# Kernel optimization log

Measured on AMD Instinct MI355X. Metric: run time of the kernel, lower is better.

## Reference

```python
import jax, jax.numpy as jnp
import numpy as np

N, E, D, H = 100000, 400000, 128, 128  # nodes, edges, feat dim, mlp hidden


def _ln(x, g, b, eps=1e-5):
    m = jnp.mean(x, axis=-1, keepdims=True)
    v = jnp.mean((x - m) ** 2, axis=-1, keepdims=True)
    return (x - m) * jax.lax.rsqrt(v + eps) * g + b


def _mlp(x, w0, b0, w1, b1, w2, b2):
    # Linear->ReLU->Linear->ReLU->Linear (last act = Identity)
    h = jax.nn.relu(x @ w0 + b0)
    h = jax.nn.relu(h @ w1 + b1)
    return h @ w2 + b2


def setup_inputs() -> dict:
    key = jax.random.key(0)
    ks = jax.random.split(key, 16)
    node_x = jax.random.normal(ks[0], (N, D), dtype=jnp.float32)
    edge_attr = jax.random.normal(ks[1], (E, D), dtype=jnp.float32)
    edge_index = jax.random.randint(ks[2], (2, E), 0, N, dtype=jnp.int32)

    def lin(k, fin, fout):
        kw, kb = jax.random.split(k)
        s = 1.0 / np.sqrt(fin)
        w = jax.random.uniform(kw, (fin, fout), jnp.float32, -s, s)
        b = jax.random.uniform(kb, (fout,), jnp.float32, -s, s)
        return w, b

    # message MLP: (3D) -> H -> H -> D, then LayerNorm(D)
    msg_w0, msg_b0 = lin(ks[3], 3 * D, H)
    msg_w1, msg_b1 = lin(ks[4], H, H)
    msg_w2, msg_b2 = lin(ks[5], H, D)
    # top-level update MLP: (D + D) -> H -> H -> D, then LayerNorm(D)
    upd_w0, upd_b0 = lin(ks[6], 2 * D, H)
    upd_w1, upd_b1 = lin(ks[7], H, H)
    upd_w2, upd_b2 = lin(ks[8], H, D)
    return {
        "node_x": node_x, "edge_attr": edge_attr, "edge_index": edge_index,
        "msg_w0": msg_w0, "msg_b0": msg_b0, "msg_w1": msg_w1, "msg_b1": msg_b1,
        "msg_w2": msg_w2, "msg_b2": msg_b2,
        "msg_g": jnp.ones((D,), jnp.float32), "msg_beta": jnp.zeros((D,), jnp.float32),
        "upd_w0": upd_w0, "upd_b0": upd_b0, "upd_w1": upd_w1, "upd_b1": upd_b1,
        "upd_w2": upd_w2, "upd_b2": upd_b2,
        "upd_g": jnp.ones((D,), jnp.float32), "upd_beta": jnp.zeros((D,), jnp.float32),
    }


def reference(node_x, edge_attr, edge_index,
              msg_w0, msg_b0, msg_w1, msg_b1, msg_w2, msg_b2, msg_g, msg_beta,
              upd_w0, upd_b0, upd_w1, upd_b1, upd_w2, upd_b2, upd_g, upd_beta):
    src, dst = edge_index[0], edge_index[1]
    # PyG default flow source_to_target: x_j = x[src], x_i = x[dst]
    x_i = node_x[dst]                       # [E, D]
    x_j = node_x[src]                       # [E, D]
    concat = jnp.concatenate([x_i, x_j, edge_attr], axis=1)  # [E, 3D]
    msg = _ln(_mlp(concat, msg_w0, msg_b0, msg_w1, msg_b1, msg_w2, msg_b2), msg_g, msg_beta)
    new_edge = edge_attr + msg              # edge_attr[:] += msg in original
    # scatter-add messages onto target nodes
    agg = jax.ops.segment_sum(new_edge, dst, num_segments=N)  # [N, D]
    concat2 = jnp.concatenate([node_x, agg], axis=1)          # [N, 2D]
    upd = _ln(_mlp(concat2, upd_w0, upd_b0, upd_w1, upd_b1, upd_w2, upd_b2), upd_g, upd_beta)
    return node_x + upd
```

## Files before the change

kernel.cpp:

```cpp
#include <hip/hip_runtime.h>

typedef __attribute__((ext_vector_type(4))) float f32x4;
typedef __attribute__((ext_vector_type(8))) __bf16 bf16x8;

constexpr int FD = 128;

__device__ __forceinline__ uint4 pack8(const float* v) {
  union { __bf16 h[8]; uint4 u; } cv;
#pragma unroll
  for (int q = 0; q < 8; ++q) cv.h[q] = (__bf16)v[q];
  return cv.u;
}
__device__ __forceinline__ unsigned int pack2(float a, float b) {
  union { __bf16 h[2]; unsigned int u; } cv;
  cv.h[0] = (__bf16)a; cv.h[1] = (__bf16)b;
  return cv.u;
}

__global__ void cvt_bf16(const float* __restrict__ x, unsigned short* __restrict__ o, int n8) {
  int i = blockIdx.x * 256 + threadIdx.x;
  if (i >= n8) return;
  const float* p = x + (size_t)i * 8;
  float v[8];
#pragma unroll
  for (int q = 0; q < 8; ++q) v[q] = p[q];
  *(uint4*)(o + (size_t)i * 8) = pack8(v);
}

__global__ void pack_weights(const float* __restrict__ mw0, const float* __restrict__ mw1,
                             const float* __restrict__ mw2, const float* __restrict__ uw0,
                             const float* __restrict__ uw1, const float* __restrict__ uw2,
                             unsigned short* __restrict__ wp) {
  int tid = blockIdx.x * 256 + threadIdx.x;
  const float* src; int base, K;
  if      (tid < 49152)  { src = mw0; base = 0;      K = 384; }
  else if (tid < 65536)  { src = mw1; base = 49152;  K = 128; }
  else if (tid < 81920)  { src = mw2; base = 65536;  K = 128; }
  else if (tid < 114688) { src = uw0; base = 81920;  K = 256; }
  else if (tid < 131072) { src = uw1; base = 114688; K = 128; }
  else                   { src = uw2; base = 131072; K = 128; }
  int i = tid - base;
  int k = i >> 7, n = i & 127;
  int KS = K >> 5;
  int dst = base + (((n >> 4) * KS + (k >> 5)) * 64 + ((k >> 3) & 3) * 16 + (n & 15)) * 8 + (k & 7);
  union { __bf16 h; unsigned short s; } cv; cv.h = (__bf16)src[i];
  wp[dst] = cv.s;
}


template<bool RELU>
__device__ __forceinline__ void store_frag(unsigned short* sDst, const f32x4* acc, float bias) {
#pragma unroll
  for (int m = 0; m < 4; ++m)
#pragma unroll
    for (int ri = 0; ri < 4; ++ri) {
      float v = acc[m][ri] + bias;
      if (RELU) v = fmaxf(v, 0.f);
      union { __bf16 h; unsigned short s; } cv; cv.h = (__bf16)v;
      sDst[m * 512 + ri * 32] = cv.s;
    }
}

__global__ __launch_bounds__(512, 6)
void in_edge_kernel(const float* __restrict__ node_x, const unsigned short* __restrict__ nxbf,
                    const float* __restrict__ edge_attr,
                    const int* __restrict__ eidx, const unsigned short* __restrict__ wp,
                    const float* __restrict__ b0p, const float* __restrict__ b1p,
                    const float* __restrict__ b2p, const float* __restrict__ gp,
                    const float* __restrict__ bep,
                    unsigned short* __restrict__ msg, int* __restrict__ head,
                    int* __restrict__ nxt, float* __restrict__ agg,
                    int use_sort, int E) {
  __shared__ unsigned short sBuf[3072 * 8];
  __shared__ int sSrc[64], sDst[64];
  __shared__ float sG[128], sB[128];

  const int t = threadIdx.x;
  const int e0 = blockIdx.x * 64;
  const int lane = t & 63, w = t >> 6;
  const int ln = lane & 15, g16 = lane >> 4;
  const int col = w * 16 + ln;
  const int rdoff = ln * 32 + g16 * 8;
  const int stoff = (w >> 1) * 2048 + g16 * 128
                  + (((2 * w) + (ln >> 3)) & 3) * 8 + (ln & 7);

  bf16x8 b0[6];
#pragma unroll
  for (int ks = 0; ks < 6; ++ks)
    b0[ks] = *(const bf16x8*)(wp + (size_t)((w * 12 + ks) * 64 + lane) * 8);
  bf16x8 B1r[4];
#pragma unroll
  for (int ks = 0; ks < 4; ++ks)
    B1r[ks] = *(const bf16x8*)(wp + 49152 + (size_t)((w * 4 + ks) * 64 + lane) * 8);

  if (t < 64) {
    sSrc[t] = (e0 + t < E) ? eidx[e0 + t] : 0;
  } else if (t < 128) {
    int r = t - 64;
    int e = e0 + r;
    int d = (e < E) ? eidx[E + e] : 0;
    sDst[r] = d;
    if (use_sort && e < E) nxt[e] = atomicExch(&head[d], e);
  } else if (t < 256) {
    sG[t - 128] = gp[t - 128];
  } else if (t < 384) {
    sB[t - 256] = bep[t - 256];
  }
  __syncthreads();

  if (nxbf) {
#pragma unroll
    for (int it = 0; it < 2; ++it) {
      int f = t + it * 512;
      int row = f >> 4, j = f & 15;
      uint4 v = {0, 0, 0, 0}, u = {0, 0, 0, 0};
      if (e0 + row < E) {
        v = *(const uint4*)(nxbf + (size_t)sDst[row] * FD + j * 8);
        u = *(const uint4*)(nxbf + (size_t)sSrc[row] * FD + j * 8);
      }
      int c = (((j >> 2) * 4 + (row >> 4)) * 64 + (row & 15) * 4 + (j & 3)) * 8;
      *(uint4*)&sBuf[c] = v;
      *(uint4*)&sBuf[c + 8192] = u;
    }
  } else {
#pragma unroll
    for (int it = 0; it < 16; ++it) {
      const int type = it >> 3;
      int row = ((it & 7) << 3) + w;
      float2 v = {0.f, 0.f};
      if (e0 + row < E) {
        const float* sp = (type == 0) ? node_x + (size_t)sDst[row] * FD
                                      : node_x + (size_t)sSrc[row] * FD;
        v = *(const float2*)(sp + lane * 2);
      }
      int c = (((type * 4 + (lane >> 4)) * 4 + (row >> 4)) * 64
               + (row & 15) * 4 + ((lane >> 2) & 3)) * 8 + (lane & 3) * 2;
      *(unsigned int*)&sBuf[c] = pack2(v.x, v.y);
    }
  }
#pragma unroll
  for (int it = 0; it < 8; ++it) {
    int row = it * 8 + w;
    float2 v = {0.f, 0.f};
    if (e0 + row < E) v = *(const float2*)(edge_attr + (size_t)(e0 + row) * FD + lane * 2);
    int c = 16384 + (((lane >> 4) * 4 + (row >> 4)) * 64
                     + (row & 15) * 4 + ((lane >> 2) & 3)) * 8 + (lane & 3) * 2;
    *(unsigned int*)&sBuf[c] = pack2(v.x, v.y);
  }
  __syncthreads();

  const float b0v = b0p[col], b1v = b1p[col], b2v = b2p[col];

  f32x4 acc[4];
#pragma unroll
  for (int m = 0; m < 4; ++m) acc[m] = (f32x4){0.f, 0.f, 0.f, 0.f};

#pragma unroll
  for (int ks = 0; ks < 12; ++ks) {
    bf16x8 bb = b0[ks % 6];
    if (ks + 6 < 12)
      b0[ks % 6] = *(const bf16x8*)(wp + (size_t)((w * 12 + ks + 6) * 64 + lane) * 8);
#pragma unroll
    for (int m = 0; m < 4; ++m) {
      bf16x8 a = *(const bf16x8*)&sBuf[(ks * 4 + m) * 512 + rdoff];
      acc[m] = __builtin_amdgcn_mfma_f32_16x16x32_bf16(a, bb, acc[m], 0, 0, 0);
    }
  }
  bf16x8 B2r[4];
#pragma unroll
  for (int ks = 0; ks < 4; ++ks)
    B2r[ks] = *(const bf16x8*)(wp + 65536 + (size_t)((w * 4 + ks) * 64 + lane) * 8);

  __syncthreads();
  store_frag<true>(sBuf + stoff, acc, b0v);
  __syncthreads();

#pragma unroll
  for (int m = 0; m < 4; ++m) acc[m] = (f32x4){0.f, 0.f, 0.f, 0.f};
#pragma unroll
  for (int ks = 0; ks < 4; ++ks)
#pragma unroll
    for (int m = 0; m < 4; ++m) {
      bf16x8 a = *(const bf16x8*)&sBuf[(ks * 4 + m) * 512 + rdoff];
      acc[m] = __builtin_amdgcn_mfma_f32_16x16x32_bf16(a, B1r[ks], acc[m], 0, 0, 0);
    }
  store_frag<true>(sBuf + 8192 + stoff, acc, b1v);
  __syncthreads();

#pragma unroll
  for (int m = 0; m < 4; ++m) acc[m] = (f32x4){0.f, 0.f, 0.f, 0.f};
#pragma unroll
  for (int ks = 0; ks < 4; ++ks)
#pragma unroll
    for (int m = 0; m < 4; ++m) {
      bf16x8 a = *(const bf16x8*)&sBuf[8192 + (ks * 4 + m) * 512 + rdoff];
      acc[m] = __builtin_amdgcn_mfma_f32_16x16x32_bf16(a, B2r[ks], acc[m], 0, 0, 0);
    }
  store_frag<false>(sBuf + stoff, acc, b2v);
  __syncthreads();

  {
    int row = t >> 3, j = t & 7;
    int a0 = (((j >> 1) * 4 + (row >> 4)) * 64 + (row & 15) * 4 + 2 * (j & 1)) * 8;
    bf16x8 v0 = *(const bf16x8*)&sBuf[a0];
    bf16x8 v1 = *(const bf16x8*)&sBuf[a0 + 8];
    float s1 = 0.f, s2 = 0.f;
#pragma unroll
    for (int q = 0; q < 8; ++q) {
      float a = (float)v0[q], b = (float)v1[q];
      s1 += a + b; s2 += a * a + b * b;
    }
#pragma unroll
    for (int m = 1; m < 8; m <<= 1) {
      s1 += __shfl_xor(s1, m, 64);
      s2 += __shfl_xor(s2, m, 64);
    }
    float mean = s1 * (1.f / 128.f);
    float var  = s2 * (1.f / 128.f) - mean * mean;
    float rstd = rsqrtf(fmaxf(var, 0.f) + 1e-5f);

    int e = e0 + row;
    if (e < E) {
      bf16x8 ea0 = *(const bf16x8*)&sBuf[a0 + 16384];
      bf16x8 ea1 = *(const bf16x8*)&sBuf[a0 + 16384 + 8];
      float val[16];
#pragma unroll
      for (int q = 0; q < 8; ++q) {
        val[q]     = ((float)v0[q] - mean) * rstd * sG[j * 16 + q]     + sB[j * 16 + q]     + (float)ea0[q];
        val[8 + q] = ((float)v1[q] - mean) * rstd * sG[j * 16 + 8 + q] + sB[j * 16 + 8 + q] + (float)ea1[q];
      }
      if (use_sort) {
        uint4* dst = (uint4*)(msg + (size_t)e * FD + j * 16);
        dst[0] = pack8(val);
        dst[1] = pack8(val + 8);
      } else {
        float* ap = agg + (size_t)sDst[row] * FD + j * 16;
#pragma unroll
        for (int q = 0; q < 16; ++q) atomicAdd(ap + q, val[q]);
      }
    }
  }
}

__global__ __launch_bounds__(512, 8)
void in_node_kernel(const float* __restrict__ node_x, const unsigned short* __restrict__ nxbf,
                    const unsigned short* __restrict__ msg, const int* __restrict__ head,
                    const int* __restrict__ nxt, const float* __restrict__ agg,
                    const unsigned short* __restrict__ wp,
                    const float* __restrict__ b0p, const float* __restrict__ b1p,
                    const float* __restrict__ b2p, const float* __restrict__ gp,
                    const float* __restrict__ bep, float* __restrict__ out,
                    int use_sort, int N) {
  __shared__ unsigned short sBuf[2048 * 8];
  __shared__ float sG[128], sB[128];

  const int t = threadIdx.x;
  const int r0 = blockIdx.x * 64;
  const int lane = t & 63, w = t >> 6;
  const int ln = lane & 15, g16 = lane >> 4;
  const int col = w * 16 + ln;
  const int rdoff = ln * 32 + g16 * 8;
  const int stoff = (w >> 1) * 2048 + g16 * 128
                  + (((2 * w) + (ln >> 3)) & 3) * 8 + (ln & 7);

  bf16x8 b0[4];
#pragma unroll
  for (int ks = 0; ks < 4; ++ks)
    b0[ks] = *(const bf16x8*)(wp + 81920 + (size_t)((w * 8 + ks) * 64 + lane) * 8);

  if (t < 128)      sG[t] = gp[t];
  else if (t < 256) sB[t - 128] = bep[t - 128];

  if (nxbf) {
#pragma unroll
    for (int it = 0; it < 2; ++it) {
      int f = t + it * 512;
      int row = f >> 4, j = f & 15;
      int r = r0 + row;
      uint4 v = {0, 0, 0, 0};
      if (r < N) v = *(const uint4*)(nxbf + (size_t)r * FD + j * 8);
      int c = (((j >> 2) * 4 + (row >> 4)) * 64 + (row & 15) * 4 + (j & 3)) * 8;
      *(uint4*)&sBuf[c] = v;
    }
  } else {
#pragma unroll
    for (int it = 0; it < 8; ++it) {
      int row = (it << 3) + w;
      int r = r0 + row;
      float2 v = {0.f, 0.f};
      if (r < N) v = *(const float2*)(node_x + (size_t)r * FD + lane * 2);
      int c = (((lane >> 4) * 4 + (row >> 4)) * 64
               + (row & 15) * 4 + ((lane >> 2) & 3)) * 8 + (lane & 3) * 2;
      *(unsigned int*)&sBuf[c] = pack2(v.x, v.y);
    }
  }

  {
    int row = t >> 3, j = t & 7;
    int node = r0 + row;
    float a[16];
#pragma unroll
    for (int q = 0; q < 16; ++q) a[q] = 0.f;
    if (node < N) {
      if (use_sort) {
        int e = head[node];
        while (e >= 0) {
          int ne = nxt[e];
          bf16x8 m0 = *(const bf16x8*)(msg + (size_t)e * FD + j * 16);
          bf16x8 m1 = *(const bf16x8*)(msg + (size_t)e * FD + j * 16 + 8);
#pragma unroll
          for (int q = 0; q < 8; ++q) { a[q] += (float)m0[q]; a[8 + q] += (float)m1[q]; }
          e = ne;
        }
      } else {
        const float* ap = agg + (size_t)node * FD + j * 16;
#pragma unroll
        for (int q4 = 0; q4 < 4; ++q4) {
          f32x4 u = *(const f32x4*)(ap + q4 * 4);
#pragma unroll
          for (int q = 0; q < 4; ++q) a[q4 * 4 + q] = u[q];
        }
      }
    }
    int c = 8192 + (((j >> 1) * 4 + (row >> 4)) * 64 + (row & 15) * 4 + 2 * (j & 1)) * 8;
    *(uint4*)&sBuf[c] = pack8(a);
    *(uint4*)&sBuf[c + 8] = pack8(a + 8);
  }
  __syncthreads();

  const float b0v = b0p[col], b1v = b1p[col], b2v = b2p[col];

  f32x4 acc[4];
#pragma unroll
  for (int m = 0; m < 4; ++m) acc[m] = (f32x4){0.f, 0.f, 0.f, 0.f};

#pragma unroll
  for (int ks = 0; ks < 8; ++ks) {
    bf16x8 bb = b0[ks % 4];
    if (ks + 4 < 8)
      b0[ks % 4] = *(const bf16x8*)(wp + 81920 + (size_t)((w * 8 + ks + 4) * 64 + lane) * 8);
#pragma unroll
    for (int m = 0; m < 4; ++m) {
      bf16x8 a = *(const bf16x8*)&sBuf[(ks * 4 + m) * 512 + rdoff];
      acc[m] = __builtin_amdgcn_mfma_f32_16x16x32_bf16(a, bb, acc[m], 0, 0, 0);
    }
  }
  bf16x8 B1r[4];
#pragma unroll
  for (int ks = 0; ks < 4; ++ks)
    B1r[ks] = *(const bf16x8*)(wp + 114688 + (size_t)((w * 4 + ks) * 64 + lane) * 8);

  __syncthreads();
  store_frag<true>(sBuf + stoff, acc, b0v);
  __syncthreads();

#pragma unroll
  for (int m = 0; m < 4; ++m) acc[m] = (f32x4){0.f, 0.f, 0.f, 0.f};
#pragma unroll
  for (int ks = 0; ks < 4; ++ks)
#pragma unroll
    for (int m = 0; m < 4; ++m) {
      bf16x8 a = *(const bf16x8*)&sBuf[(ks * 4 + m) * 512 + rdoff];
      acc[m] = __builtin_amdgcn_mfma_f32_16x16x32_bf16(a, B1r[ks], acc[m], 0, 0, 0);
    }
  bf16x8 B2r[4];
#pragma unroll
  for (int ks = 0; ks < 4; ++ks)
    B2r[ks] = *(const bf16x8*)(wp + 131072 + (size_t)((w * 4 + ks) * 64 + lane) * 8);
  store_frag<true>(sBuf + 8192 + stoff, acc, b1v);
  __syncthreads();

#pragma unroll
  for (int m = 0; m < 4; ++m) acc[m] = (f32x4){0.f, 0.f, 0.f, 0.f};
#pragma unroll
  for (int ks = 0; ks < 4; ++ks)
#pragma unroll
    for (int m = 0; m < 4; ++m) {
      bf16x8 a = *(const bf16x8*)&sBuf[8192 + (ks * 4 + m) * 512 + rdoff];
      acc[m] = __builtin_amdgcn_mfma_f32_16x16x32_bf16(a, B2r[ks], acc[m], 0, 0, 0);
    }
  store_frag<false>(sBuf + stoff, acc, b2v);
  __syncthreads();

  {
    int row = t >> 3, j = t & 7;
    int a0 = (((j >> 1) * 4 + (row >> 4)) * 64 + (row & 15) * 4 + 2 * (j & 1)) * 8;
    bf16x8 v0 = *(const bf16x8*)&sBuf[a0];
    bf16x8 v1 = *(const bf16x8*)&sBuf[a0 + 8];
    float s1 = 0.f, s2 = 0.f;
#pragma unroll
    for (int q = 0; q < 8; ++q) {
      float a = (float)v0[q], b = (float)v1[q];
      s1 += a + b; s2 += a * a + b * b;
    }
#pragma unroll
    for (int m = 1; m < 8; m <<= 1) {
      s1 += __shfl_xor(s1, m, 64);
      s2 += __shfl_xor(s2, m, 64);
    }
    float mean = s1 * (1.f / 128.f);
    float var  = s2 * (1.f / 128.f) - mean * mean;
    float rstd = rsqrtf(fmaxf(var, 0.f) + 1e-5f);

    int node = r0 + row;
    if (node < N) {
      float o[16];
#pragma unroll
      for (int q = 0; q < 8; ++q) {
        o[q]     = ((float)v0[q] - mean) * rstd * sG[j * 16 + q]     + sB[j * 16 + q];
        o[8 + q] = ((float)v1[q] - mean) * rstd * sG[j * 16 + 8 + q] + sB[j * 16 + 8 + q];
      }
      const float* xr = node_x + (size_t)node * FD + j * 16;
      float* orow = out + (size_t)node * FD + j * 16;
#pragma unroll
      for (int q4 = 0; q4 < 4; ++q4) {
        f32x4 x = *(const f32x4*)(xr + q4 * 4);
        f32x4 wv;
#pragma unroll
        for (int q = 0; q < 4; ++q) wv[q] = o[q4 * 4 + q] + x[q];
        *(f32x4*)(orow + q4 * 4) = wv;
      }
    }
  }
}

extern "C" void kernel_launch(void* const* d_in, const int* in_sizes, int n_in,
                              void* d_out, int out_size, void* d_ws, size_t ws_size,
                              hipStream_t stream) {
  const float* node_x    = (const float*)d_in[0];
  const float* edge_attr = (const float*)d_in[1];
  const int*   eidx      = (const int*)d_in[2];
  const int N = in_sizes[0] / FD;
  const int E = in_sizes[1] / FD;

  char* ws = (char*)d_ws;
  auto aln = [](size_t x) { return (x + 255) & ~(size_t)255; };
  const size_t wpB   = aln(294912);
  const size_t nxbfB = aln((size_t)N * FD * 2);
  const size_t headB = aln((size_t)N * 4);
  const size_t nxtB  = aln((size_t)E * 4);
  const size_t msgB  = (size_t)E * FD * 2;

  unsigned short* wp = (unsigned short*)ws;
  unsigned short* nxbf = nullptr;
  int* head = nullptr; int* nxt = nullptr;
  unsigned short* msg = nullptr; float* agg = nullptr;
  int use_sort = 0;

  if (ws_size >= wpB + nxbfB + headB + nxtB + msgB) {
    use_sort = 1;
    nxbf = (unsigned short*)(ws + wpB);
    head = (int*)(ws + wpB + nxbfB);
    nxt  = (int*)(ws + wpB + nxbfB + headB);
    msg  = (unsigned short*)(ws + wpB + nxbfB + headB + nxtB);
  } else if (ws_size >= wpB + headB + nxtB + msgB) {
    use_sort = 1;
    head = (int*)(ws + wpB);
    nxt  = (int*)(ws + wpB + headB);
    msg  = (unsigned short*)(ws + wpB + headB + nxtB);
  } else {
    agg = (float*)(ws + wpB);
  }

  if (use_sort) (void)hipMemsetAsync(head, 0xFF, (size_t)N * 4, stream);
  else          (void)hipMemsetAsync(agg, 0, (size_t)N * FD * sizeof(float), stream);

  pack_weights<<<576, 256, 0, stream>>>(
      (const float*)d_in[3], (const float*)d_in[5], (const float*)d_in[7],
      (const float*)d_in[11], (const float*)d_in[13], (const float*)d_in[15], wp);
  if (nxbf) cvt_bf16<<<(N * FD / 8 + 255) / 256, 256, 0, stream>>>(node_x, nxbf, N * FD / 8);
  in_edge_kernel<<<(E + 63) / 64, 512, 0, stream>>>(
      node_x, nxbf, edge_attr, eidx, wp,
      (const float*)d_in[4], (const float*)d_in[6], (const float*)d_in[8],
      (const float*)d_in[9], (const float*)d_in[10],
      msg, head, nxt, agg, use_sort, E);
  in_node_kernel<<<(N + 63) / 64, 512, 0, stream>>>(
      node_x, nxbf, msg, head, nxt, agg, wp,
      (const float*)d_in[12], (const float*)d_in[14], (const float*)d_in[16],
      (const float*)d_in[17], (const float*)d_in[18], (float*)d_out, use_sort, N);
}
```

Baseline: 239.4 us.

## Swizzle edge-kernel LDS layout, widen gathers, shrink weight prefetch, raise MFMA priority

Measured after the change: 300.1 us. 1.25x slower.

```diff
diff --git a/kernel.cpp b/kernel.cpp
--- a/kernel.cpp
+++ b/kernel.cpp
@@ -11,10 +11,11 @@
   for (int q = 0; q < 8; ++q) cv.h[q] = (__bf16)v[q];
   return cv.u;
 }
-__device__ __forceinline__ unsigned int pack2(float a, float b) {
-  union { __bf16 h[2]; unsigned int u; } cv;
-  cv.h[0] = (__bf16)a; cv.h[1] = (__bf16)b;
-  return cv.u;
+__device__ __forceinline__ uint4 pack8v(const f32x4 a, const f32x4 b) {
+  float v[8];
+#pragma unroll
+  for (int q = 0; q < 4; ++q) { v[q] = a[q]; v[4 + q] = b[q]; }
+  return pack8(v);
 }
 
 __global__ void cvt_bf16(const float* __restrict__ x, unsigned short* __restrict__ o, int n8) {
@@ -48,19 +49,6 @@
 }
 
 
-template<bool RELU>
-__device__ __forceinline__ void store_frag(unsigned short* sDst, const f32x4* acc, float bias) {
-#pragma unroll
-  for (int m = 0; m < 4; ++m)
-#pragma unroll
-    for (int ri = 0; ri < 4; ++ri) {
-      float v = acc[m][ri] + bias;
-      if (RELU) v = fmaxf(v, 0.f);
-      union { __bf16 h; unsigned short s; } cv; cv.h = (__bf16)v;
-      sDst[m * 512 + ri * 32] = cv.s;
-    }
-}
-
 __global__ __launch_bounds__(512, 6)
 void in_edge_kernel(const float* __restrict__ node_x, const unsigned short* __restrict__ nxbf,
                     const float* __restrict__ edge_attr,
@@ -79,19 +67,17 @@
   const int e0 = blockIdx.x * 64;
   const int lane = t & 63, w = t >> 6;
   const int ln = lane & 15, g16 = lane >> 4;
-  const int col = w * 16 + ln;
-  const int rdoff = ln * 32 + g16 * 8;
-  const int stoff = (w >> 1) * 2048 + g16 * 128
-                  + (((2 * w) + (ln >> 3)) & 3) * 8 + (ln & 7);
-
-  bf16x8 b0[6];
-#pragma unroll
-  for (int ks = 0; ks < 6; ++ks)
-    b0[ks] = *(const bf16x8*)(wp + (size_t)((w * 12 + ks) * 64 + lane) * 8);
-  bf16x8 B1r[4];
-#pragma unroll
-  for (int ks = 0; ks < 4; ++ks)
-    B1r[ks] = *(const bf16x8*)(wp + 49152 + (size_t)((w * 4 + ks) * 64 + lane) * 8);
+  const int ql = ln * 4 + g16;
+  const int keyw = (w >> 1) & 3;
+  const int stoffX = g16 * 128 + ((((2 * w) + (ln >> 3)) & 3) ^ keyw) * 8 + (ln & 7);
+
+  bf16x8 bx[4], B1r[4];
+#pragma unroll
+  for (int k = 0; k < 4; ++k)
+    bx[k] = *(const bf16x8*)(wp + (size_t)((w * 12 + k) * 64 + lane) * 8);
+#pragma unroll
+  for (int k = 0; k < 4; ++k)
+    B1r[k] = *(const bf16x8*)(wp + 49152 + (size_t)((w * 4 + k) * 64 + lane) * 8);
 
   if (t < 64) {
     sSrc[t] = (e0 + t < E) ? eidx[e0 + t] : 0;
@@ -109,101 +95,146 @@
   __syncthreads();
 
   if (nxbf) {
+    int sel = w >> 2;
+    int row = (w * 16 + (lane >> 2)) & 63;
+    int tt = lane & 3;
+    const int* idxp = sel ? sSrc : sDst;
+    uint4 v[4] = {{0,0,0,0},{0,0,0,0},{0,0,0,0},{0,0,0,0}};
+    if (e0 + row < E) {
+      const unsigned short* sp = nxbf + (size_t)idxp[row] * FD + tt * 32;
+#pragma unroll
+      for (int i = 0; i < 4; ++i) v[i] = *(const uint4*)(sp + i * 8);
+    }
+    int grp = tt * 4 + (row >> 4);
+    int base = sel * 8192 + grp * 512 + (row & 15) * 32;
+#pragma unroll
+    for (int i = 0; i < 4; ++i)
+      *(uint4*)&sBuf[base + ((i ^ tt) * 8)] = v[i];
+  } else {
 #pragma unroll
     for (int it = 0; it < 2; ++it) {
-      int f = t + it * 512;
-      int row = f >> 4, j = f & 15;
-      uint4 v = {0, 0, 0, 0}, u = {0, 0, 0, 0};
+      int sel = w >> 2;
+      int row = (w * 16 + (lane >> 2)) & 63;
+      int seg = (lane & 3) + it * 4;
+      const int* idxp = sel ? sSrc : sDst;
+      f32x4 f[4] = {{0,0,0,0},{0,0,0,0},{0,0,0,0},{0,0,0,0}};
       if (e0 + row < E) {
-        v = *(const uint4*)(nxbf + (size_t)sDst[row] * FD + j * 8);
-        u = *(const uint4*)(nxbf + (size_t)sSrc[row] * FD + j * 8);
-      }
-      int c = (((j >> 2) * 4 + (row >> 4)) * 64 + (row & 15) * 4 + (j & 3)) * 8;
-      *(uint4*)&sBuf[c] = v;
-      *(uint4*)&sBuf[c + 8192] = u;
-    }
-  } else {
-#pragma unroll
-    for (int it = 0; it < 16; ++it) {
-      const int type = it >> 3;
-      int row = ((it & 7) << 3) + w;
-      float2 v = {0.f, 0.f};
-      if (e0 + row < E) {
-        const float* sp = (type == 0) ? node_x + (size_t)sDst[row] * FD
-                                      : node_x + (size_t)sSrc[row] * FD;
-        v = *(const float2*)(sp + lane * 2);
-      }
-      int c = (((type * 4 + (lane >> 4)) * 4 + (row >> 4)) * 64
-               + (row & 15) * 4 + ((lane >> 2) & 3)) * 8 + (lane & 3) * 2;
-      *(unsigned int*)&sBuf[c] = pack2(v.x, v.y);
-    }
-  }
-#pragma unroll
-  for (int it = 0; it < 8; ++it) {
-    int row = it * 8 + w;
-    float2 v = {0.f, 0.f};
-    if (e0 + row < E) v = *(const float2*)(edge_attr + (size_t)(e0 + row) * FD + lane * 2);
-    int c = 16384 + (((lane >> 4) * 4 + (row >> 4)) * 64
-                     + (row & 15) * 4 + ((lane >> 2) & 3)) * 8 + (lane & 3) * 2;
-    *(unsigned int*)&sBuf[c] = pack2(v.x, v.y);
-  }
-  __syncthreads();
-
+        const float* sp = node_x + (size_t)idxp[row] * FD + seg * 16;
+#pragma unroll
+        for (int i = 0; i < 4; ++i) f[i] = *(const f32x4*)(sp + i * 4);
+      }
+      int jc = seg * 2;
+      int grp = (jc >> 2) * 4 + (row >> 4);
+      int key = (grp >> 2) & 3;
+      int tb = sel * 8192 + grp * 512;
+      int q0 = (row & 15) * 4 + (jc & 3);
+      *(uint4*)&sBuf[tb + ((q0 ^ key) * 8)]       = pack8v(f[0], f[1]);
+      *(uint4*)&sBuf[tb + (((q0 + 1) ^ key) * 8)] = pack8v(f[2], f[3]);
+    }
+  }
+  {
+    int row = t >> 3, seg = t & 7;
+    f32x4 f[4] = {{0,0,0,0},{0,0,0,0},{0,0,0,0},{0,0,0,0}};
+    if (e0 + row < E) {
+      const float* sp = edge_attr + (size_t)(e0 + row) * FD + seg * 16;
+#pragma unroll
+      for (int i = 0; i < 4; ++i) f[i] = *(const f32x4*)(sp + i * 4);
+    }
+    int jc = seg * 2;
+    int grp = (jc >> 2) * 4 + (row >> 4);
+    int key = (grp >> 2) & 3;
+    int tb = 16384 + grp * 512;
+    int q0 = (row & 15) * 4 + (jc & 3);
+    *(uint4*)&sBuf[tb + ((q0 ^ key) * 8)]       = pack8v(f[0], f[1]);
+    *(uint4*)&sBuf[tb + (((q0 + 1) ^ key) * 8)] = pack8v(f[2], f[3]);
+  }
+  __syncthreads();
+
+  const int col = w * 16 + ln;
   const float b0v = b0p[col], b1v = b1p[col], b2v = b2p[col];
 
   f32x4 acc[4];
 #pragma unroll
   for (int m = 0; m < 4; ++m) acc[m] = (f32x4){0.f, 0.f, 0.f, 0.f};
 
+  __builtin_amdgcn_s_setprio(1);
 #pragma unroll
   for (int ks = 0; ks < 12; ++ks) {
-    bf16x8 bb = b0[ks % 6];
-    if (ks + 6 < 12)
-      b0[ks % 6] = *(const bf16x8*)(wp + (size_t)((w * 12 + ks + 6) * 64 + lane) * 8);
+    bf16x8 bb = bx[ks & 3];
+    if (ks + 4 < 12)
+      bx[ks & 3] = *(const bf16x8*)(wp + (size_t)((w * 12 + ks + 4) * 64 + lane) * 8);
 #pragma unroll
     for (int m = 0; m < 4; ++m) {
-      bf16x8 a = *(const bf16x8*)&sBuf[(ks * 4 + m) * 512 + rdoff];
+      bf16x8 a = *(const bf16x8*)&sBuf[(ks * 4 + m) * 512 + ((ql ^ (ks & 3)) * 8)];
       acc[m] = __builtin_amdgcn_mfma_f32_16x16x32_bf16(a, bb, acc[m], 0, 0, 0);
     }
   }
-  bf16x8 B2r[4];
-#pragma unroll
-  for (int ks = 0; ks < 4; ++ks)
-    B2r[ks] = *(const bf16x8*)(wp + 65536 + (size_t)((w * 4 + ks) * 64 + lane) * 8);
-
-  __syncthreads();
-  store_frag<true>(sBuf + stoff, acc, b0v);
-  __syncthreads();
-
-#pragma unroll
-  for (int m = 0; m < 4; ++m) acc[m] = (f32x4){0.f, 0.f, 0.f, 0.f};
+  __builtin_amdgcn_s_setprio(0);
+#pragma unroll
+  for (int k = 0; k < 4; ++k)
+    bx[k] = *(const bf16x8*)(wp + 65536 + (size_t)((w * 4 + k) * 64 + lane) * 8);
+  __syncthreads();
+
+#pragma unroll
+  for (int m = 0; m < 4; ++m)
+#pragma unroll
+    for (int ri = 0; ri < 4; ++ri) {
+      union { __bf16 h; unsigned short s; } cv;
+      cv.h = (__bf16)fmaxf(acc[m][ri] + b0v, 0.f);
+      sBuf[((w >> 1) * 4 + m) * 512 + ri * 32 + stoffX] = cv.s;
+      acc[m][ri] = 0.f;
+    }
+  __syncthreads();
+
+  __builtin_amdgcn_s_setprio(1);
 #pragma unroll
   for (int ks = 0; ks < 4; ++ks)
 #pragma unroll
     for (int m = 0; m < 4; ++m) {
-      bf16x8 a = *(const bf16x8*)&sBuf[(ks * 4 + m) * 512 + rdoff];
+      bf16x8 a = *(const bf16x8*)&sBuf[(ks * 4 + m) * 512 + ((ql ^ ks) * 8)];
       acc[m] = __builtin_amdgcn_mfma_f32_16x16x32_bf16(a, B1r[ks], acc[m], 0, 0, 0);
     }
-  store_frag<true>(sBuf + 8192 + stoff, acc, b1v);
-  __syncthreads();
-
-#pragma unroll
-  for (int m = 0; m < 4; ++m) acc[m] = (f32x4){0.f, 0.f, 0.f, 0.f};
+  __builtin_amdgcn_s_setprio(0);
+#pragma unroll
+  for (int m = 0; m < 4; ++m)
+#pragma unroll
+    for (int ri = 0; ri < 4; ++ri) {
+      union { __bf16 h; unsigned short s; } cv;
+      cv.h = (__bf16)fmaxf(acc[m][ri] + b1v, 0.f);
+      sBuf[8192 + ((w >> 1) * 4 + m) * 512 + ri * 32 + stoffX] = cv.s;
+      acc[m][ri] = 0.f;
+    }
+  __syncthreads();
+
+  __builtin_amdgcn_s_setprio(1);
 #pragma unroll
   for (int ks = 0; ks < 4; ++ks)
 #pragma unroll
     for (int m = 0; m < 4; ++m) {
-      bf16x8 a = *(const bf16x8*)&sBuf[8192 + (ks * 4 + m) * 512 + rdoff];
-      acc[m] = __builtin_amdgcn_mfma_f32_16x16x32_bf16(a, B2r[ks], acc[m], 0, 0, 0);
-    }
-  store_frag<false>(sBuf + stoff, acc, b2v);
+      bf16x8 a = *(const bf16x8*)&sBuf[8192 + (ks * 4 + m) * 512 + ((ql ^ ks) * 8)];
+      acc[m] = __builtin_amdgcn_mfma_f32_16x16x32_bf16(a, bx[ks], acc[m], 0, 0, 0);
+    }
+  __builtin_amdgcn_s_setprio(0);
+#pragma unroll
+  for (int m = 0; m < 4; ++m)
+#pragma unroll
+    for (int ri = 0; ri < 4; ++ri) {
+      union { __bf16 h; unsigned short s; } cv;
+      cv.h = (__bf16)(acc[m][ri] + b2v);
+      sBuf[((w >> 1) * 4 + m) * 512 + ri * 32 + stoffX] = cv.s;
+    }
   __syncthreads();
 
   {
     int row = t >> 3, j = t & 7;
-    int a0 = (((j >> 1) * 4 + (row >> 4)) * 64 + (row & 15) * 4 + 2 * (j & 1)) * 8;
+    int grp = (j >> 1) * 4 + (row >> 4);
+    int key = (j >> 1) & 3;
+    int qa = ((row & 15) * 4 + 2 * (j & 1)) ^ key;
+    int qb = ((row & 15) * 4 + 2 * (j & 1) + 1) ^ key;
+    int a0 = grp * 512 + qa * 8;
+    int a1 = grp * 512 + qb * 8;
     bf16x8 v0 = *(const bf16x8*)&sBuf[a0];
-    bf16x8 v1 = *(const bf16x8*)&sBuf[a0 + 8];
+    bf16x8 v1 = *(const bf16x8*)&sBuf[a1];
     float s1 = 0.f, s2 = 0.f;
 #pragma unroll
     for (int q = 0; q < 8; ++q) {
@@ -221,8 +252,8 @@
 
     int e = e0 + row;
     if (e < E) {
-      bf16x8 ea0 = *(const bf16x8*)&sBuf[a0 + 16384];
-      bf16x8 ea1 = *(const bf16x8*)&sBuf[a0 + 16384 + 8];
+      bf16x8 ea0 = *(const bf16x8*)&sBuf[16384 + a0];
+      bf16x8 ea1 = *(const bf16x8*)&sBuf[16384 + a1];
       float val[16];
 #pragma unroll
       for (int q = 0; q < 8; ++q) {
@@ -284,14 +315,17 @@
     }
   } else {
 #pragma unroll
-    for (int it = 0; it < 8; ++it) {
-      int row = (it << 3) + w;
+    for (int it = 0; it < 2; ++it) {
+      int f = t + it * 512;
+      int row = f >> 4, j = f & 15;
       int r = r0 + row;
-      float2 v = {0.f, 0.f};
-      if (r < N) v = *(const float2*)(node_x + (size_t)r * FD + lane * 2);
-      int c = (((lane >> 4) * 4 + (row >> 4)) * 64
-               + (row & 15) * 4 + ((lane >> 2) & 3)) * 8 + (lane & 3) * 2;
-      *(unsigned int*)&sBuf[c] = pack2(v.x, v.y);
+      f32x4 fa = {0,0,0,0}, fb = {0,0,0,0};
+      if (r < N) {
+        fa = *(const f32x4*)(node_x + (size_t)r * FD + j * 8);
+        fb = *(const f32x4*)(node_x + (size_t)r * FD + j * 8 + 4);
+      }
+      int c = (((j >> 2) * 4 + (row >> 4)) * 64 + (row & 15) * 4 + (j & 3)) * 8;
+      *(uint4*)&sBuf[c] = pack8v(fa, fb);
     }
   }
 
@@ -351,11 +385,17 @@
     B1r[ks] = *(const bf16x8*)(wp + 114688 + (size_t)((w * 4 + ks) * 64 + lane) * 8);
 
   __syncthreads();
-  store_frag<true>(sBuf + stoff, acc, b0v);
-  __syncthreads();
-
-#pragma unroll
-  for (int m = 0; m < 4; ++m) acc[m] = (f32x4){0.f, 0.f, 0.f, 0.f};
+#pragma unroll
+  for (int m = 0; m < 4; ++m)
+#pragma unroll
+    for (int ri = 0; ri < 4; ++ri) {
+      union { __bf16 h; unsigned short s; } cv;
+      cv.h = (__bf16)fmaxf(acc[m][ri] + b0v, 0.f);
+      sBuf[stoff + m * 512 + ri * 32] = cv.s;
+      acc[m][ri] = 0.f;
+    }
+  __syncthreads();
+
 #pragma unroll
   for (int ks = 0; ks < 4; ++ks)
 #pragma unroll
@@ -367,11 +407,17 @@
 #pragma unroll
   for (int ks = 0; ks < 4; ++ks)
     B2r[ks] = *(const bf16x8*)(wp + 131072 + (size_t)((w * 4 + ks) * 64 + lane) * 8);
-  store_frag<true>(sBuf + 8192 + stoff, acc, b1v);
-  __syncthreads();
-
-#pragma unroll
-  for (int m = 0; m < 4; ++m) acc[m] = (f32x4){0.f, 0.f, 0.f, 0.f};
+#pragma unroll
+  for (int m = 0; m < 4; ++m)
+#pragma unroll
+    for (int ri = 0; ri < 4; ++ri) {
+      union { __bf16 h; unsigned short s; } cv;
+      cv.h = (__bf16)fmaxf(acc[m][ri] + b1v, 0.f);
+      sBuf[8192 + stoff + m * 512 + ri * 32] = cv.s;
+      acc[m][ri] = 0.f;
+    }
+  __syncthreads();
+
 #pragma unroll
   for (int ks = 0; ks < 4; ++ks)
 #pragma unroll
@@ -379,7 +425,14 @@
       bf16x8 a = *(const bf16x8*)&sBuf[8192 + (ks * 4 + m) * 512 + rdoff];
       acc[m] = __builtin_amdgcn_mfma_f32_16x16x32_bf16(a, B2r[ks], acc[m], 0, 0, 0);
     }
-  store_frag<false>(sBuf + stoff, acc, b2v);
+#pragma unroll
+  for (int m = 0; m < 4; ++m)
+#pragma unroll
+    for (int ri = 0; ri < 4; ++ri) {
+      union { __bf16 h; unsigned short s; } cv;
+      cv.h = (__bf16)(acc[m][ri] + b2v);
+      sBuf[stoff + m * 512 + ri * 32] = cv.s;
+    }
   __syncthreads();
 
   {
```

## Restructure edge MLP as register-resident swapped GEMM with shuffle-based layer transitions

Applied to the files above, without the earlier changes.

Result: slower. 424.7 us (+77.4%).

```diff
diff --git a/kernel.cpp b/kernel.cpp
--- a/kernel.cpp
+++ b/kernel.cpp
@@ -2,20 +2,26 @@
 
 typedef __attribute__((ext_vector_type(4))) float f32x4;
 typedef __attribute__((ext_vector_type(8))) __bf16 bf16x8;
+typedef unsigned int u32;
 
 constexpr int FD = 128;
 
+__device__ __forceinline__ u32 pk2(float a, float b) {
+  union { __bf16 h[2]; u32 u; } cv; cv.h[0] = (__bf16)a; cv.h[1] = (__bf16)b; return cv.u;
+}
+__device__ __forceinline__ bf16x8 mk8(u32 a, u32 b, u32 c, u32 d) {
+  union { u32 w[4]; bf16x8 v; } cv; cv.w[0] = a; cv.w[1] = b; cv.w[2] = c; cv.w[3] = d; return cv.v;
+}
+__device__ __forceinline__ bf16x8 pack8f(const f32x4 a, const f32x4 b) {
+  return mk8(pk2(a[0], a[1]), pk2(a[2], a[3]), pk2(b[0], b[1]), pk2(b[2], b[3]));
+}
 __device__ __forceinline__ uint4 pack8(const float* v) {
   union { __bf16 h[8]; uint4 u; } cv;
 #pragma unroll
   for (int q = 0; q < 8; ++q) cv.h[q] = (__bf16)v[q];
   return cv.u;
 }
-__device__ __forceinline__ unsigned int pack2(float a, float b) {
-  union { __bf16 h[2]; unsigned int u; } cv;
-  cv.h[0] = (__bf16)a; cv.h[1] = (__bf16)b;
-  return cv.u;
-}
+__device__ __forceinline__ unsigned int pack2(float a, float b) { return pk2(a, b); }
 
 __global__ void cvt_bf16(const float* __restrict__ x, unsigned short* __restrict__ o, int n8) {
   int i = blockIdx.x * 256 + threadIdx.x;
@@ -47,21 +53,7 @@
   wp[dst] = cv.s;
 }
 
-
-template<bool RELU>
-__device__ __forceinline__ void store_frag(unsigned short* sDst, const f32x4* acc, float bias) {
-#pragma unroll
-  for (int m = 0; m < 4; ++m)
-#pragma unroll
-    for (int ri = 0; ri < 4; ++ri) {
-      float v = acc[m][ri] + bias;
-      if (RELU) v = fmaxf(v, 0.f);
-      union { __bf16 h; unsigned short s; } cv; cv.h = (__bf16)v;
-      sDst[m * 512 + ri * 32] = cv.s;
-    }
-}
-
-__global__ __launch_bounds__(512, 6)
+__global__ __launch_bounds__(256, 4)
 void in_edge_kernel(const float* __restrict__ node_x, const unsigned short* __restrict__ nxbf,
                     const float* __restrict__ edge_attr,
                     const int* __restrict__ eidx, const unsigned short* __restrict__ wp,
@@ -71,172 +63,173 @@
                     unsigned short* __restrict__ msg, int* __restrict__ head,
                     int* __restrict__ nxt, float* __restrict__ agg,
                     int use_sort, int E) {
-  __shared__ unsigned short sBuf[3072 * 8];
-  __shared__ int sSrc[64], sDst[64];
-  __shared__ float sG[128], sB[128];
+  __shared__ float sP[5][128];
 
   const int t = threadIdx.x;
-  const int e0 = blockIdx.x * 64;
   const int lane = t & 63, w = t >> 6;
   const int ln = lane & 15, g16 = lane >> 4;
-  const int col = w * 16 + ln;
-  const int rdoff = ln * 32 + g16 * 8;
-  const int stoff = (w >> 1) * 2048 + g16 * 128
-                  + (((2 * w) + (ln >> 3)) & 3) * 8 + (ln & 7);
-
-  bf16x8 b0[6];
-#pragma unroll
-  for (int ks = 0; ks < 6; ++ks)
-    b0[ks] = *(const bf16x8*)(wp + (size_t)((w * 12 + ks) * 64 + lane) * 8);
-  bf16x8 B1r[4];
-#pragma unroll
-  for (int ks = 0; ks < 4; ++ks)
-    B1r[ks] = *(const bf16x8*)(wp + 49152 + (size_t)((w * 4 + ks) * 64 + lane) * 8);
-
-  if (t < 64) {
-    sSrc[t] = (e0 + t < E) ? eidx[e0 + t] : 0;
-  } else if (t < 128) {
-    int r = t - 64;
-    int e = e0 + r;
-    int d = (e < E) ? eidx[E + e] : 0;
-    sDst[r] = d;
-    if (use_sort && e < E) nxt[e] = atomicExch(&head[d], e);
-  } else if (t < 256) {
-    sG[t - 128] = gp[t - 128];
-  } else if (t < 384) {
-    sB[t - 256] = bep[t - 256];
-  }
-  __syncthreads();
-
-  if (nxbf) {
-#pragma unroll
-    for (int it = 0; it < 2; ++it) {
-      int f = t + it * 512;
-      int row = f >> 4, j = f & 15;
-      uint4 v = {0, 0, 0, 0}, u = {0, 0, 0, 0};
-      if (e0 + row < E) {
-        v = *(const uint4*)(nxbf + (size_t)sDst[row] * FD + j * 8);
-        u = *(const uint4*)(nxbf + (size_t)sSrc[row] * FD + j * 8);
-      }
-      int c = (((j >> 2) * 4 + (row >> 4)) * 64 + (row & 15) * 4 + (j & 3)) * 8;
-      *(uint4*)&sBuf[c] = v;
-      *(uint4*)&sBuf[c + 8192] = u;
-    }
-  } else {
-#pragma unroll
-    for (int it = 0; it < 16; ++it) {
-      const int type = it >> 3;
-      int row = ((it & 7) << 3) + w;
-      float2 v = {0.f, 0.f};
-      if (e0 + row < E) {
-        const float* sp = (type == 0) ? node_x + (size_t)sDst[row] * FD
-                                      : node_x + (size_t)sSrc[row] * FD;
-        v = *(const float2*)(sp + lane * 2);
-      }
-      int c = (((type * 4 + (lane >> 4)) * 4 + (row >> 4)) * 64
-               + (row & 15) * 4 + ((lane >> 2) & 3)) * 8 + (lane & 3) * 2;
-      *(unsigned int*)&sBuf[c] = pack2(v.x, v.y);
-    }
-  }
-#pragma unroll
-  for (int it = 0; it < 8; ++it) {
-    int row = it * 8 + w;
-    float2 v = {0.f, 0.f};
-    if (e0 + row < E) v = *(const float2*)(edge_attr + (size_t)(e0 + row) * FD + lane * 2);
-    int c = 16384 + (((lane >> 4) * 4 + (row >> 4)) * 64
-                     + (row & 15) * 4 + ((lane >> 2) & 3)) * 8 + (lane & 3) * 2;
-    *(unsigned int*)&sBuf[c] = pack2(v.x, v.y);
-  }
-  __syncthreads();
-
-  const float b0v = b0p[col], b1v = b1p[col], b2v = b2p[col];
-
-  f32x4 acc[4];
-#pragma unroll
-  for (int m = 0; m < 4; ++m) acc[m] = (f32x4){0.f, 0.f, 0.f, 0.f};
-
-#pragma unroll
-  for (int ks = 0; ks < 12; ++ks) {
-    bf16x8 bb = b0[ks % 6];
-    if (ks + 6 < 12)
-      b0[ks % 6] = *(const bf16x8*)(wp + (size_t)((w * 12 + ks + 6) * 64 + lane) * 8);
-#pragma unroll
-    for (int m = 0; m < 4; ++m) {
-      bf16x8 a = *(const bf16x8*)&sBuf[(ks * 4 + m) * 512 + rdoff];
-      acc[m] = __builtin_amdgcn_mfma_f32_16x16x32_bf16(a, bb, acc[m], 0, 0, 0);
-    }
-  }
-  bf16x8 B2r[4];
-#pragma unroll
-  for (int ks = 0; ks < 4; ++ks)
-    B2r[ks] = *(const bf16x8*)(wp + 65536 + (size_t)((w * 4 + ks) * 64 + lane) * 8);
-
-  __syncthreads();
-  store_frag<true>(sBuf + stoff, acc, b0v);
-  __syncthreads();
-
-#pragma unroll
-  for (int m = 0; m < 4; ++m) acc[m] = (f32x4){0.f, 0.f, 0.f, 0.f};
-#pragma unroll
-  for (int ks = 0; ks < 4; ++ks)
-#pragma unroll
-    for (int m = 0; m < 4; ++m) {
-      bf16x8 a = *(const bf16x8*)&sBuf[(ks * 4 + m) * 512 + rdoff];
-      acc[m] = __builtin_amdgcn_mfma_f32_16x16x32_bf16(a, B1r[ks], acc[m], 0, 0, 0);
-    }
-  store_frag<true>(sBuf + 8192 + stoff, acc, b1v);
-  __syncthreads();
-
-#pragma unroll
-  for (int m = 0; m < 4; ++m) acc[m] = (f32x4){0.f, 0.f, 0.f, 0.f};
-#pragma unroll
-  for (int ks = 0; ks < 4; ++ks)
-#pragma unroll
-    for (int m = 0; m < 4; ++m) {
-      bf16x8 a = *(const bf16x8*)&sBuf[8192 + (ks * 4 + m) * 512 + rdoff];
-      acc[m] = __builtin_amdgcn_mfma_f32_16x16x32_bf16(a, B2r[ks], acc[m], 0, 0, 0);
-    }
-  store_frag<false>(sBuf + stoff, acc, b2v);
-  __syncthreads();
-
-  {
-    int row = t >> 3, j = t & 7;
-    int a0 = (((j >> 1) * 4 + (row >> 4)) * 64 + (row & 15) * 4 + 2 * (j & 1)) * 8;
-    bf16x8 v0 = *(const bf16x8*)&sBuf[a0];
-    bf16x8 v1 = *(const bf16x8*)&sBuf[a0 + 8];
-    float s1 = 0.f, s2 = 0.f;
-#pragma unroll
-    for (int q = 0; q < 8; ++q) {
-      float a = (float)v0[q], b = (float)v1[q];
-      s1 += a + b; s2 += a * a + b * b;
-    }
-#pragma unroll
-    for (int m = 1; m < 8; m <<= 1) {
-      s1 += __shfl_xor(s1, m, 64);
-      s2 += __shfl_xor(s2, m, 64);
-    }
-    float mean = s1 * (1.f / 128.f);
-    float var  = s2 * (1.f / 128.f) - mean * mean;
-    float rstd = rsqrtf(fmaxf(var, 0.f) + 1e-5f);
-
-    int e = e0 + row;
-    if (e < E) {
-      bf16x8 ea0 = *(const bf16x8*)&sBuf[a0 + 16384];
-      bf16x8 ea1 = *(const bf16x8*)&sBuf[a0 + 16384 + 8];
-      float val[16];
-#pragma unroll
-      for (int q = 0; q < 8; ++q) {
-        val[q]     = ((float)v0[q] - mean) * rstd * sG[j * 16 + q]     + sB[j * 16 + q]     + (float)ea0[q];
-        val[8 + q] = ((float)v1[q] - mean) * rstd * sG[j * 16 + 8 + q] + sB[j * 16 + 8 + q] + (float)ea1[q];
-      }
-      if (use_sort) {
-        uint4* dst = (uint4*)(msg + (size_t)e * FD + j * 16);
-        dst[0] = pack8(val);
-        dst[1] = pack8(val + 8);
-      } else {
-        float* ap = agg + (size_t)sDst[row] * FD + j * 16;
-#pragma unroll
-        for (int q = 0; q < 16; ++q) atomicAdd(ap + q, val[q]);
+  const int e0w = blockIdx.x * 128 + w * 32;
+  const int erow0 = e0w + ln, erow1 = e0w + 16 + ln;
+  const int kg = 8 * g16;
+
+  int si0 = 0, si1 = 0, di0 = 0, di1 = 0;
+  if (erow0 < E) { si0 = eidx[erow0]; di0 = eidx[E + erow0]; }
+  if (erow1 < E) { si1 = eidx[erow1]; di1 = eidx[E + erow1]; }
+
+  if (t < 128) {
+    sP[0][t] = b0p[t]; sP[1][t] = b1p[t]; sP[2][t] = b2p[t];
+    sP[3][t] = gp[t];  sP[4][t] = bep[t];
+  }
+  if (use_sort && lane < 32) {
+    int e = e0w + lane;
+    if (e < E) { int d = (lane < 16) ? di0 : di1; nxt[e] = atomicExch(&head[d], e); }
+  }
+  __syncthreads();
+
+  auto xf = [&](int idx, int ko) -> bf16x8 {
+    if (nxbf) return *(const bf16x8*)(nxbf + (size_t)idx * FD + ko);
+    f32x4 a = *(const f32x4*)(node_x + (size_t)idx * FD + ko);
+    f32x4 b = *(const f32x4*)(node_x + (size_t)idx * FD + ko + 4);
+    return pack8f(a, b);
+  };
+  auto eaf = [&](int row, int ko) -> bf16x8 {
+    f32x4 a = {0.f,0.f,0.f,0.f}, b = {0.f,0.f,0.f,0.f};
+    if (row < E) {
+      a = *(const f32x4*)(edge_attr + (size_t)row * FD + ko);
+      b = *(const f32x4*)(edge_attr + (size_t)row * FD + ko + 4);
+    }
+    return pack8f(a, b);
+  };
+
+  bf16x8 rb[4][2];
+  auto loadkb = [&](int kb) {
+    int s = kb & 3;
+    if (kb < 4)      { int ko = kb * 32 + kg;       rb[s][0] = xf(di0, ko);     rb[s][1] = xf(di1, ko); }
+    else if (kb < 8) { int ko = (kb - 4) * 32 + kg; rb[s][0] = xf(si0, ko);     rb[s][1] = xf(si1, ko); }
+    else             { int ko = (kb - 8) * 32 + kg; rb[s][0] = eaf(erow0, ko);  rb[s][1] = eaf(erow1, ko); }
+  };
+
+  f32x4 acc[8][2];
+#pragma unroll
+  for (int mb = 0; mb < 8; ++mb)
+#pragma unroll
+    for (int nb = 0; nb < 2; ++nb) acc[mb][nb] = (f32x4){0.f, 0.f, 0.f, 0.f};
+
+  loadkb(0); loadkb(1); loadkb(2);
+
+#pragma unroll
+  for (int kb = 0; kb < 12; ++kb) {
+    if (kb + 3 < 12) loadkb(kb + 3);
+    const int s = kb & 3;
+#pragma unroll
+    for (int mb = 0; mb < 8; ++mb) {
+      bf16x8 a = *(const bf16x8*)(wp + (size_t)((mb * 12 + kb) * 64 + lane) * 8);
+      acc[mb][0] = __builtin_amdgcn_mfma_f32_16x16x32_bf16(a, rb[s][0], acc[mb][0], 0, 0, 0);
+      acc[mb][1] = __builtin_amdgcn_mfma_f32_16x16x32_bf16(a, rb[s][1], acc[mb][1], 0, 0, 0);
+    }
+  }
+
+  const int s0l = ln + ((g16 & 1) << 5);
+  const int s1l = s0l + 16;
+  const bool hi = g16 >= 2;
+  bf16x8 Bn[4][2];
+
+  auto transition = [&](int lyr) {
+    u32 clo[8][2], chi[8][2];
+#pragma unroll
+    for (int mb = 0; mb < 8; ++mb) {
+      f32x4 bv = *(const f32x4*)&sP[lyr][mb * 16 + 4 * g16];
+#pragma unroll
+      for (int nb = 0; nb < 2; ++nb) {
+        float v0 = fmaxf(acc[mb][nb][0] + bv[0], 0.f);
+        float v1 = fmaxf(acc[mb][nb][1] + bv[1], 0.f);
+        float v2 = fmaxf(acc[mb][nb][2] + bv[2], 0.f);
+        float v3 = fmaxf(acc[mb][nb][3] + bv[3], 0.f);
+        clo[mb][nb] = pk2(v0, v1); chi[mb][nb] = pk2(v2, v3);
+      }
+    }
+#pragma unroll
+    for (int kb = 0; kb < 4; ++kb)
+#pragma unroll
+      for (int nb = 0; nb < 2; ++nb) {
+        u32 a0 = __shfl((int)clo[2 * kb][nb], s0l, 64),     a1 = __shfl((int)chi[2 * kb][nb], s0l, 64);
+        u32 a2 = __shfl((int)clo[2 * kb][nb], s1l, 64),     a3 = __shfl((int)chi[2 * kb][nb], s1l, 64);
+        u32 b0 = __shfl((int)clo[2 * kb + 1][nb], s0l, 64), b1 = __shfl((int)chi[2 * kb + 1][nb], s0l, 64);
+        u32 b2 = __shfl((int)clo[2 * kb + 1][nb], s1l, 64), b3 = __shfl((int)chi[2 * kb + 1][nb], s1l, 64);
+        Bn[kb][nb] = mk8(hi ? b0 : a0, hi ? b1 : a1, hi ? b2 : a2, hi ? b3 : a3);
+      }
+#pragma unroll
+    for (int mb = 0; mb < 8; ++mb)
+#pragma unroll
+      for (int nb = 0; nb < 2; ++nb) acc[mb][nb] = (f32x4){0.f, 0.f, 0.f, 0.f};
+  };
+
+  transition(0);
+
+#pragma unroll
+  for (int kb = 0; kb < 4; ++kb)
+#pragma unroll
+    for (int mb = 0; mb < 8; ++mb) {
+      bf16x8 a = *(const bf16x8*)(wp + 49152 + (size_t)((mb * 4 + kb) * 64 + lane) * 8);
+      acc[mb][0] = __builtin_amdgcn_mfma_f32_16x16x32_bf16(a, Bn[kb][0], acc[mb][0], 0, 0, 0);
+      acc[mb][1] = __builtin_amdgcn_mfma_f32_16x16x32_bf16(a, Bn[kb][1], acc[mb][1], 0, 0, 0);
+    }
+
+  transition(1);
+
+#pragma unroll
+  for (int kb = 0; kb < 4; ++kb)
+#pragma unroll
+    for (int mb = 0; mb < 8; ++mb) {
+      bf16x8 a = *(const bf16x8*)(wp + 65536 + (size_t)((mb * 4 + kb) * 64 + lane) * 8);
+      acc[mb][0] = __builtin_amdgcn_mfma_f32_16x16x32_bf16(a, Bn[kb][0], acc[mb][0], 0, 0, 0);
+      acc[mb][1] = __builtin_amdgcn_mfma_f32_16x16x32_bf16(a, Bn[kb][1], acc[mb][1], 0, 0, 0);
+    }
+
+  float mean[2], rstd[2];
+#pragma unroll
+  for (int nb = 0; nb < 2; ++nb) {
+    float p = 0.f, q = 0.f;
+#pragma unroll
+    for (int mb = 0; mb < 8; ++mb) {
+      f32x4 bv = *(const f32x4*)&sP[2][mb * 16 + 4 * g16];
+#pragma unroll
+      for (int r = 0; r < 4; ++r) {
+        float v = acc[mb][nb][r] + bv[r];
+        acc[mb][nb][r] = v;
+        p += v; q += v * v;
+      }
+    }
+    p += __shfl_xor(p, 16, 64); p += __shfl_xor(p, 32, 64);
+    q += __shfl_xor(q, 16, 64); q += __shfl_xor(q, 32, 64);
+    float m_ = p * (1.f / 128.f);
+    float var = q * (1.f / 128.f) - m_ * m_;
+    mean[nb] = m_;
+    rstd[nb] = rsqrtf(fmaxf(var, 0.f) + 1e-5f);
+  }
+
+#pragma unroll
+  for (int mb = 0; mb < 8; ++mb) {
+    f32x4 gv  = *(const f32x4*)&sP[3][mb * 16 + 4 * g16];
+    f32x4 bev = *(const f32x4*)&sP[4][mb * 16 + 4 * g16];
+#pragma unroll
+    for (int nb = 0; nb < 2; ++nb) {
+      int row = nb ? erow1 : erow0;
+      if (row < E) {
+        f32x4 ea = *(const f32x4*)(edge_attr + (size_t)row * FD + mb * 16 + 4 * g16);
+        float v0 = (acc[mb][nb][0] - mean[nb]) * rstd[nb] * gv[0] + bev[0] + ea[0];
+        float v1 = (acc[mb][nb][1] - mean[nb]) * rstd[nb] * gv[1] + bev[1] + ea[1];
+        float v2 = (acc[mb][nb][2] - mean[nb]) * rstd[nb] * gv[2] + bev[2] + ea[2];
+        float v3 = (acc[mb][nb][3] - mean[nb]) * rstd[nb] * gv[3] + bev[3] + ea[3];
+        if (use_sort) {
+          uint2 o; o.x = pk2(v0, v1); o.y = pk2(v2, v3);
+          *(uint2*)(msg + (size_t)row * FD + mb * 16 + 4 * g16) = o;
+        } else {
+          int d = nb ? di1 : di0;
+          float* ap = agg + (size_t)d * FD + mb * 16 + 4 * g16;
+          atomicAdd(ap + 0, v0); atomicAdd(ap + 1, v1);
+          atomicAdd(ap + 2, v2); atomicAdd(ap + 3, v3);
+        }
       }
     }
   }
@@ -323,8 +316,9 @@
       }
     }
     int c = 8192 + (((j >> 1) * 4 + (row >> 4)) * 64 + (row & 15) * 4 + 2 * (j & 1)) * 8;
-    *(uint4*)&sBuf[c] = pack8(a);
-    *(uint4*)&sBuf[c + 8] = pack8(a + 8);
+    float* ap2 = a;
+    *(uint4*)&sBuf[c] = pack8(ap2);
+    *(uint4*)&sBuf[c + 8] = pack8(ap2 + 8);
   }
   __syncthreads();
 
@@ -351,11 +345,17 @@
     B1r[ks] = *(const bf16x8*)(wp + 114688 + (size_t)((w * 4 + ks) * 64 + lane) * 8);
 
   __syncthreads();
-  store_frag<true>(sBuf + stoff, acc, b0v);
-  __syncthreads();
-
-#pragma unroll
-  for (int m = 0; m < 4; ++m) acc[m] = (f32x4){0.f, 0.f, 0.f, 0.f};
+#pragma unroll
+  for (int m = 0; m < 4; ++m)
+#pragma unroll
+    for (int ri = 0; ri < 4; ++ri) {
+      union { __bf16 h; unsigned short s; } cv;
+      cv.h = (__bf16)fmaxf(acc[m][ri] + b0v, 0.f);
+      sBuf[stoff + m * 512 + ri * 32] = cv.s;
+      acc[m][ri] = 0.f;
+    }
+  __syncthreads();
+
 #pragma unroll
   for (int ks = 0; ks < 4; ++ks)
 #pragma unroll
@@ -367,11 +367,17 @@
 #pragma unroll
   for (int ks = 0; ks < 4; ++ks)
     B2r[ks] = *(const bf16x8*)(wp + 131072 + (size_t)((w * 4 + ks) * 64 + lane) * 8);
-  store_frag<true>(sBuf + 8192 + stoff, acc, b1v);
-  __syncthreads();
-
-#pragma unroll
-  for (int m = 0; m < 4; ++m) acc[m] = (f32x4){0.f, 0.f, 0.f, 0.f};
+#pragma unroll
+  for (int m = 0; m < 4; ++m)
+#pragma unroll
+    for (int ri = 0; ri < 4; ++ri) {
+      union { __bf16 h; unsigned short s; } cv;
+      cv.h = (__bf16)fmaxf(acc[m][ri] + b1v, 0.f);
+      sBuf[8192 + stoff + m * 512 + ri * 32] = cv.s;
+      acc[m][ri] = 0.f;
+    }
+  __syncthreads();
+
 #pragma unroll
   for (int ks = 0; ks < 4; ++ks)
 #pragma unroll
@@ -379,7 +385,14 @@
       bf16x8 a = *(const bf16x8*)&sBuf[8192 + (ks * 4 + m) * 512 + rdoff];
       acc[m] = __builtin_amdgcn_mfma_f32_16x16x32_bf16(a, B2r[ks], acc[m], 0, 0, 0);
     }
-  store_frag<false>(sBuf + stoff, acc, b2v);
+#pragma unroll
+  for (int m = 0; m < 4; ++m)
+#pragma unroll
+    for (int ri = 0; ri < 4; ++ri) {
+      union { __bf16 h; unsigned short s; } cv;
+      cv.h = (__bf16)(acc[m][ri] + b2v);
+      sBuf[stoff + m * 512 + ri * 32] = cv.s;
+    }
   __syncthreads();
 
   {
@@ -469,7 +482,7 @@
       (const float*)d_in[3], (const float*)d_in[5], (const float*)d_in[7],
       (const float*)d_in[11], (const float*)d_in[13], (const float*)d_in[15], wp);
   if (nxbf) cvt_bf16<<<(N * FD / 8 + 255) / 256, 256, 0, stream>>>(node_x, nxbf, N * FD / 8);
-  in_edge_kernel<<<(E + 63) / 64, 512, 0, stream>>>(
+  in_edge_kernel<<<(E + 127) / 128, 256, 0, stream>>>(
       node_x, nxbf, edge_attr, eidx, wp,
       (const float*)d_in[4], (const float*)d_in[6], (const float*)d_in[8],
       (const float*)d_in[9], (const float*)d_in[10],
```
